# Kernel optimization log

Measured on AMD Instinct MI355X. Metric: run time of the kernel, lower is better.

Reference implementation:

```python
import jax, jax.numpy as jnp
import numpy as np

B, C, P, L = 128, 5, 5, 5
D = 128
USER_NUM, TITLE_NUM, ENTITY_NUM, REL_NUM = 50000, 30000, 100000, 100


def setup_inputs() -> dict:
    key = jax.random.key(0)
    k = jax.random.split(key, 22)
    f = jnp.float32
    s = 0.1  # weight scale to keep LSTM gates in a sane range
    return {
        "candidate_newsindex": jax.random.randint(k[0], (B, C), 0, TITLE_NUM),
        "user_index": jax.random.randint(k[1], (B,), 0, USER_NUM),
        "total_paths_index": jax.random.randint(k[2], (USER_NUM, C, P, L), 0, TITLE_NUM),
        "total_type_index": jax.random.randint(k[3], (USER_NUM, C, P, L), 0, 3),
        "total_relations_index": jax.random.randint(k[4], (USER_NUM, C, P, L), 0, REL_NUM),
        "entity_emb": jax.random.normal(k[5], (ENTITY_NUM, D), f),
        "relation_emb": jax.random.normal(k[6], (REL_NUM, D), f),
        "user_emb": jax.random.normal(k[7], (USER_NUM, D), f),
        "news_emb": jax.random.normal(k[8], (TITLE_NUM, D), f),
        "type_emb": jax.random.normal(k[9], (3, D), f),
        "Wih0": jax.random.normal(k[10], (P, 4 * D, 3 * D), f) * s,
        "Whh0": jax.random.normal(k[11], (P, 4 * D, D), f) * s,
        "bih0": jax.random.normal(k[12], (P, 4 * D), f) * s,
        "bhh0": jax.random.normal(k[13], (P, 4 * D), f) * s,
        "Wih1": jax.random.normal(k[14], (P, 4 * D, D), f) * s,
        "Whh1": jax.random.normal(k[15], (P, 4 * D, D), f) * s,
        "bih1": jax.random.normal(k[16], (P, 4 * D), f) * s,
        "bhh1": jax.random.normal(k[17], (P, 4 * D), f) * s,
        "W1": jax.random.normal(k[18], (16, D), f) * s,
        "b1": jax.random.normal(k[19], (16,), f) * s,
        "W2": jax.random.normal(k[20], (1, 16), f) * s,
        "b2": jax.random.normal(k[21], (1,), f) * s,
    }


def _lstm2(x, Wih0, Whh0, bih0, bhh0, Wih1, Whh1, bih1, bhh1):
    """2-layer PyTorch-style LSTM (gate order i,f,g,o). x: [N, T, in] -> [N, T, H]."""
    def layer(x, Wih, Whh, bih, bhh):
        N = x.shape[0]
        H = Whh.shape[1]
        h0 = jnp.zeros((N, H), x.dtype)
        c0 = jnp.zeros((N, H), x.dtype)
        b = bih + bhh
        def step(carry, xt):
            h, c = carry
            g = xt @ Wih.T + h @ Whh.T + b
            i, f, gg, o = jnp.split(g, 4, axis=-1)
            c = jax.nn.sigmoid(f) * c + jax.nn.sigmoid(i) * jnp.tanh(gg)
            h = jax.nn.sigmoid(o) * jnp.tanh(c)
            return (h, c), h
        _, ys = jax.lax.scan(step, (h0, c0), x.swapaxes(0, 1))
        return ys.swapaxes(0, 1)
    x = layer(x, Wih0, Whh0, bih0, bhh0)
    x = layer(x, Wih1, Whh1, bih1, bhh1)
    return x


def reference(candidate_newsindex, user_index, total_paths_index, total_type_index,
              total_relations_index, entity_emb, relation_emb, user_emb, news_emb,
              type_emb, Wih0, Whh0, bih0, bhh0, Wih1, Whh1, bih1, bhh1,
              W1, b1, W2, b2):
    bpath = total_paths_index[user_index]  # [B,C,P,L]
    btype = total_type_index[user_index]
    brel = total_relations_index[user_index]
    # per-node embedding selected by type: 0->user, 1->news, else entity
    node = jnp.where((btype == 0)[..., None], user_emb[bpath],
                     jnp.where((btype == 1)[..., None], news_emb[bpath], entity_emb[bpath]))
    inp = jnp.concatenate([node, type_emb[btype], relation_emb[brel]], axis=-1)  # [B,C,P,L,3D]
    Bb, Cc, Pp, Ll, F = inp.shape
    x = inp.transpose(2, 0, 1, 3, 4).reshape(Pp, Bb * Cc, Ll, F)  # per-path batches
    outs = jax.vmap(_lstm2)(x, Wih0, Whh0, bih0, bhh0, Wih1, Whh1, bih1, bhh1)  # [P,BC,L,H]
    idx = jnp.arange(Pp)
    sel = outs[idx, :, idx, :]  # LSTM i's output at timestep i -> [P, BC, H]
    ps = jax.nn.sigmoid(jnp.maximum(sel @ W1.T + b1, 0.0) @ W2.T + b2)[..., 0]  # [P,BC]
    ps_mean = ps.reshape(Pp, Bb, Cc).mean(axis=0)  # [B,C]
    # faithful to source: total_output accumulates over candidates j, so the score
    # for candidate j is the cumulative mean of path scores for candidates 0..j
    total_score = jnp.cumsum(ps_mean, axis=1) / jnp.arange(1, Cc + 1, dtype=ps_mean.dtype)
    emb_score = jax.nn.sigmoid(jnp.sum(news_emb[candidate_newsindex] * user_emb[user_index][:, None, :], axis=-1))
    return emb_score + total_score
```

## Files before the change

kernel.cpp:

```cpp
#include <hip/hip_runtime.h>
#include <math.h>

#define BB   128
#define CC   5
#define PP   5
#define LL   5
#define DD   128
#define NSEQ 640
#define GATES 512
#define IN0  384
#define HPAD 136

typedef __attribute__((ext_vector_type(8))) short short8;
typedef __attribute__((ext_vector_type(4))) float f32x4;

__device__ __forceinline__ float sigf(float x){ return 1.0f/(1.0f+__expf(-x)); }
__device__ __forceinline__ float tanhfast(float x){ return 1.0f - 2.0f/(__expf(2.0f*x)+1.0f); }

__device__ __forceinline__ unsigned short f2bf(float x){
    union { float f; unsigned u; } v; v.f = x;
    unsigned r = v.u + 0x7FFF + ((v.u >> 16) & 1);
    return (unsigned short)(r >> 16);
}

__device__ __constant__ int c_ptmap[15] = {0,5,6,10,11,12,15,16,17,18,20,21,22,23,24};

__global__ void stage0_kernel(const float* __restrict__ Wih0, const float* __restrict__ Whh0,
                              const float* __restrict__ Wih1, const float* __restrict__ Whh1,
                              const float* __restrict__ bih0, const float* __restrict__ bhh0,
                              const float* __restrict__ bih1, const float* __restrict__ bhh1,
                              unsigned short* __restrict__ F0, unsigned short* __restrict__ F1,
                              unsigned short* __restrict__ F2, unsigned short* __restrict__ F3,
                              float* __restrict__ b0, float* __restrict__ b1c,
                              float* __restrict__ psum,
                              const int* __restrict__ user_index,
                              const int* __restrict__ tpath, const int* __restrict__ ttype,
                              const int* __restrict__ trel,
                              const float* __restrict__ entity_emb, const float* __restrict__ relation_emb,
                              const float* __restrict__ user_emb, const float* __restrict__ news_emb,
                              const float* __restrict__ type_emb,
                              unsigned short* __restrict__ X){
    int bx = blockIdx.x;
    if (bx < 985){
        int id = bx*256 + threadIdx.x;
        const int NF0 = PP*12*32*64;
        const int NFH = PP*4*32*64;
        if (id < NF0 + 3*NFH){
            const float* src; unsigned short* dst; int K, KT, fid;
            if (id < NF0){ src = Wih0; dst = F0; K = IN0; KT = 12; fid = id; }
            else {
                int j = id - NF0; int m = j / NFH; fid = j % NFH; K = DD; KT = 4;
                src = (m==0)?Whh0:(m==1)?Wih1:Whh1;
                dst = (m==0)?F1:(m==1)?F2:F3;
            }
            int lane = fid & 63; int rem = fid >> 6;
            int gt = rem & 31; rem >>= 5;
            int kt = rem % KT; int p = rem / KT;
            int g  = gt*16 + (lane & 15);
            int k0 = kt*32 + (lane >> 4)*8;
            const float* s = src + (size_t)(p*GATES + g)*K + k0;
            float4 x0 = *(const float4*)s;
            float4 x1 = *(const float4*)(s+4);
            uint4 o;
            o.x = f2bf(x0.x) | ((unsigned)f2bf(x0.y)<<16);
            o.y = f2bf(x0.z) | ((unsigned)f2bf(x0.w)<<16);
            o.z = f2bf(x1.x) | ((unsigned)f2bf(x1.y)<<16);
            o.w = f2bf(x1.z) | ((unsigned)f2bf(x1.w)<<16);
            *(uint4*)(dst + (size_t)fid*8) = o;
        } else {
            int j = id - (NF0 + 3*NFH);
            if (j < PP*GATES) b0[j] = bih0[j] + bhh0[j];
            else if (j < 2*PP*GATES){ int q = j - PP*GATES; b1c[q] = bih1[q] + bhh1[q]; }
            else if (j < 2*PP*GATES + NSEQ){ psum[j - 2*PP*GATES] = 0.0f; }
        }
    } else {
        int id = (bx - 985)*256 + threadIdx.x;
        if (id >= 15*NSEQ*48) return;
        int ptIdx = id / (NSEQ*48); int rem = id % (NSEQ*48);
        int n = rem / 48, q = rem % 48;
        int pt = c_ptmap[ptIdx];
        int p = pt / LL, t = pt % LL;
        int b = n / CC, c = n % CC;
        int u = user_index[b];
        int base = ((u*CC + c)*PP + p)*LL + t;
        int col = q*8;
        const float* s;
        if (q < 16){
            int ty = ttype[base]; int pi = tpath[base];
            const float* e = (ty==0)?user_emb:(ty==1)?news_emb:entity_emb;
            s = e + (size_t)pi*DD + col;
        } else if (q < 32){
            s = type_emb + (size_t)ttype[base]*DD + (col-128);
        } else {
            s = relation_emb + (size_t)trel[base]*DD + (col-256);
        }
        float4 x0 = *(const float4*)s, x1 = *(const float4*)(s+4);
        uint4 o;
        o.x = f2bf(x0.x) | ((unsigned)f2bf(x0.y)<<16);
        o.y = f2bf(x0.z) | ((unsigned)f2bf(x0.w)<<16);
        o.z = f2bf(x1.x) | ((unsigned)f2bf(x1.y)<<16);
        o.w = f2bf(x1.z) | ((unsigned)f2bf(x1.w)<<16);
        *(uint4*)(X + (size_t)(pt*NSEQ + n)*IN0 + col) = o;
    }
}

__global__ __launch_bounds__(256) void gemm_ih0_v5(const unsigned short* __restrict__ X,
                                                   const unsigned short* __restrict__ F0,
                                                   float* __restrict__ G0c){
    __shared__ unsigned short Bs[12*4*512];
    int bx = blockIdx.x;
    int nch = bx & 7;
    int m64 = (bx >> 3) % 10;
    int pt  = c_ptmap[bx / 80];
    int p = pt / LL;
    int tid = threadIdx.x, lane = tid & 63, w = tid >> 6;
    int r16 = lane & 15, qd = lane >> 4;

    const unsigned short* Fp = F0 + (((size_t)p*12)*32 + nch*4)*512;
    uint4 breg[12];
    #pragma unroll
    for (int j=0;j<12;j++)
        breg[j] = *(const uint4*)(Fp + (size_t)j*32*512 + tid*8);
    #pragma unroll
    for (int j=0;j<12;j++)
        *(uint4*)(Bs + j*2048 + tid*8) = breg[j];
    __syncthreads();

    f32x4 acc[4];
    #pragma unroll
    for (int i=0;i<4;i++) acc[i] = (f32x4)0.0f;
    const unsigned short* Xb = X + ((size_t)pt*NSEQ + m64*64 + w*16 + r16)*IN0 + qd*8;
    #pragma unroll
    for (int kt=0; kt<12; kt++){
        short8 a = *(const short8*)(Xb + kt*32);
        #pragma unroll
        for (int i=0;i<4;i++){
            short8 bfr = *(const short8*)(Bs + (kt*4+i)*512 + lane*8);
            acc[i] = __builtin_amdgcn_mfma_f32_16x16x32_bf16(a, bfr, acc[i], 0,0,0);
        }
    }
    int tile16 = pt*40 + m64*4 + w;
    float* dst = G0c + (((size_t)tile16*32 + nch*4)*64 + lane)*4;
    #pragma unroll
    for (int i=0;i<4;i++)
        *(f32x4*)(dst + (size_t)i*256) = acc[i];
}

__global__ __launch_bounds__(512) void lstm_v5(
    const float* __restrict__ G0c,
    const unsigned short* __restrict__ F1,
    const unsigned short* __restrict__ F2,
    const unsigned short* __restrict__ F3,
    const float* __restrict__ b0, const float* __restrict__ b1c,
    const float* __restrict__ W1, const float* __restrict__ b1v,
    const float* __restrict__ W2, const float* __restrict__ b2v,
    float* __restrict__ psum){
    __shared__ unsigned short h0T[16*HPAD];
    __shared__ unsigned short h1T[16*HPAD];
    __shared__ float h1f[16*132];
    __shared__ float mlpb[16*17];

    int p = blockIdx.x / 40, nt = blockIdx.x % 40;
    int n0 = nt*16;
    int tid = threadIdx.x;
    int lane = tid & 63, w = tid >> 6;
    int r16 = lane & 15, qd = lane >> 4;
    int j = w*16 + r16;

    short8 f2r[16], f3r[16];
    {
        const unsigned short* F2p = F2 + (size_t)p*4*32*512 + lane*8;
        const unsigned short* F3p = F3 + (size_t)p*4*32*512 + lane*8;
        #pragma unroll
        for (int kt=0; kt<4; kt++)
            #pragma unroll
            for (int i=0;i<4;i++){
                f2r[kt*4+i] = *(const short8*)(F2p + (size_t)(kt*32 + i*8 + w)*512);
                f3r[kt*4+i] = *(const short8*)(F3p + (size_t)(kt*32 + i*8 + w)*512);
            }
    }
    float bL0[4], bL1[4];
    #pragma unroll
    for (int i=0;i<4;i++){
        int col = (i*8 + w)*16 + r16;
        bL0[i] = b0[p*GATES + col];
        bL1[i] = b1c[p*GATES + col];
    }
    const unsigned short* F1p = F1 + (size_t)p*4*32*512 + lane*8;

    f32x4 pf[4];
    {
        const float* slab = G0c + (size_t)((p*LL + 0)*40 + nt)*8192;
        #pragma unroll
        for (int i=0;i<4;i++) pf[i] = *(const f32x4*)(slab + ((i*8+w)*64 + lane)*4);
    }
    float c0s[4] = {0,0,0,0}, c1s[4] = {0,0,0,0};

    for (int t=0; t<=p; t++){
        f32x4 acc[4];
        #pragma unroll
        for (int i=0;i<4;i++){
            f32x4 a = pf[i]; float bb = bL0[i];
            a[0]+=bb; a[1]+=bb; a[2]+=bb; a[3]+=bb; acc[i]=a;
        }
        if (t < p){
            const float* ns = G0c + (size_t)((p*LL + t + 1)*40 + nt)*8192;
            #pragma unroll
            for (int i=0;i<4;i++) pf[i] = *(const f32x4*)(ns + ((i*8+w)*64 + lane)*4);
        }
        if (t > 0){
            #pragma unroll
            for (int kt=0; kt<4; kt++){
                short8 a = *(const short8*)(h0T + r16*HPAD + kt*32 + qd*8);
                #pragma unroll
                for (int i=0;i<4;i++){
                    short8 bfr = *(const short8*)(F1p + (size_t)(kt*32 + i*8 + w)*512);
                    acc[i] = __builtin_amdgcn_mfma_f32_16x16x32_bf16(a, bfr, acc[i], 0,0,0);
                }
            }
        }
        __syncthreads();
        #pragma unroll
        for (int v=0; v<4; v++){
            float cc = sigf(acc[1][v])*c0s[v] + sigf(acc[0][v])*tanhfast(acc[2][v]);
            c0s[v] = cc;
            h0T[(qd*4+v)*HPAD + j] = f2bf(sigf(acc[3][v])*tanhfast(cc));
        }
        __syncthreads();
        #pragma unroll
        for (int i=0;i<4;i++){
            float bb = bL1[i];
            f32x4 a; a[0]=bb; a[1]=bb; a[2]=bb; a[3]=bb; acc[i]=a;
        }
        #pragma unroll
        for (int kt=0; kt<4; kt++){
            short8 a = *(const short8*)(h0T + r16*HPAD + kt*32 + qd*8);
            #pragma unroll
            for (int i=0;i<4;i++)
                acc[i] = __builtin_amdgcn_mfma_f32_16x16x32_bf16(a, f2r[kt*4+i], acc[i], 0,0,0);
        }
        if (t > 0){
            #pragma unroll
            for (int kt=0; kt<4; kt++){
                short8 a = *(const short8*)(h1T + r16*HPAD + kt*32 + qd*8);
                #pragma unroll
                for (int i=0;i<4;i++)
                    acc[i] = __builtin_amdgcn_mfma_f32_16x16x32_bf16(a, f3r[kt*4+i], acc[i], 0,0,0);
            }
        }
        __syncthreads();
        #pragma unroll
        for (int v=0; v<4; v++){
            float cc = sigf(acc[1][v])*c1s[v] + sigf(acc[0][v])*tanhfast(acc[2][v]);
            c1s[v] = cc;
            float hh = sigf(acc[3][v])*tanhfast(cc);
            if (t < p) h1T[(qd*4+v)*HPAD + j] = f2bf(hh);
            else       h1f[(qd*4+v)*132 + j] = hh;
        }
    }
    __syncthreads();
    if (tid < 256){
        int rr = tid & 15, hc = tid >> 4;
        const float* w1r = W1 + hc*DD;
        float acc = b1v[hc];
        #pragma unroll 4
        for (int k=0;k<DD;k++) acc = fmaf(h1f[rr*132 + k], w1r[k], acc);
        mlpb[hc*17 + rr] = fmaxf(acc, 0.0f);
    }
    __syncthreads();
    if (tid < 16){
        float s = b2v[0];
        #pragma unroll
        for (int h=0;h<16;h++) s = fmaf(mlpb[h*17 + tid], W2[h], s);
        atomicAdd(&psum[n0 + tid], 0.2f*sigf(s));
    }
}

__global__ void final_kernel(const int* __restrict__ cand, const int* __restrict__ user_index,
                             const float* __restrict__ news_emb, const float* __restrict__ user_emb,
                             const float* __restrict__ psum, float* __restrict__ out){
    int b = blockIdx.x;
    int lane = threadIdx.x;
    int u = user_index[b];
    const float* ue = user_emb + (size_t)u*DD;
    float cum = 0.0f;
    for (int c=0;c<CC;c++){
        int nb = cand[b*CC + c];
        const float* ne = news_emb + (size_t)nb*DD;
        float v = ne[lane]*ue[lane] + ne[lane+64]*ue[lane+64];
        #pragma unroll
        for (int off=32; off; off>>=1) v += __shfl_down(v, off, 64);
        if (lane == 0){
            cum += psum[b*CC + c];
            out[b*CC + c] = sigf(v) + cum/(float)(c+1);
        }
    }
}

extern "C" void kernel_launch(void* const* d_in, const int* in_sizes, int n_in,
                              void* d_out, int out_size, void* d_ws, size_t ws_size,
                              hipStream_t stream){
    const int* cand        = (const int*)d_in[0];
    const int* uidx        = (const int*)d_in[1];
    const int* tpath       = (const int*)d_in[2];
    const int* ttype       = (const int*)d_in[3];
    const int* trel        = (const int*)d_in[4];
    const float* entity_emb   = (const float*)d_in[5];
    const float* relation_emb = (const float*)d_in[6];
    const float* user_emb     = (const float*)d_in[7];
    const float* news_emb     = (const float*)d_in[8];
    const float* type_emb     = (const float*)d_in[9];
    const float* Wih0 = (const float*)d_in[10];
    const float* Whh0 = (const float*)d_in[11];
    const float* bih0 = (const float*)d_in[12];
    const float* bhh0 = (const float*)d_in[13];
    const float* Wih1 = (const float*)d_in[14];
    const float* Whh1 = (const float*)d_in[15];
    const float* bih1 = (const float*)d_in[16];
    const float* bhh1 = (const float*)d_in[17];
    const float* W1 = (const float*)d_in[18];
    const float* b1 = (const float*)d_in[19];
    const float* W2 = (const float*)d_in[20];
    const float* b2 = (const float*)d_in[21];
    float* out = (float*)d_out;

    char* ws = (char*)d_ws;
    unsigned short* F0 = (unsigned short*)ws;  ws += (size_t)PP*12*32*512*2;
    unsigned short* F1 = (unsigned short*)ws;  ws += (size_t)PP*4*32*512*2;
    unsigned short* F2 = (unsigned short*)ws;  ws += (size_t)PP*4*32*512*2;
    unsigned short* F3 = (unsigned short*)ws;  ws += (size_t)PP*4*32*512*2;
    float* b0  = (float*)ws;                   ws += PP*GATES*4;
    float* b1c = (float*)ws;                   ws += PP*GATES*4;
    unsigned short* X = (unsigned short*)ws;   ws += (size_t)PP*LL*NSEQ*IN0*2;
    float* G0c = (float*)ws;                   ws += (size_t)PP*LL*NSEQ*GATES*4;
    float* psum = (float*)ws;                  ws += NSEQ*4;

    stage0_kernel<<<985+1800,256,0,stream>>>(Wih0,Whh0,Wih1,Whh1,bih0,bhh0,bih1,bhh1,
                                             F0,F1,F2,F3,b0,b1c,psum,
                                             uidx,tpath,ttype,trel,entity_emb,relation_emb,
                                             user_emb,news_emb,type_emb,X);
    gemm_ih0_v5<<<1200,256,0,stream>>>(X, F0, G0c);
    lstm_v5<<<200,512,0,stream>>>(G0c, F1, F2, F3, b0, b1c, W1, b1, W2, b2, psum);
    final_kernel<<<BB,64,0,stream>>>(cand, uidx, news_emb, user_emb, psum, out);
}
```

Before: 233.9 us.

## Double-buffer LSTM hidden state, cache F1 in registers, fuse final kernel

Result: slower. 351.2 us (+50.1%).

```diff
diff --git a/kernel.cpp b/kernel.cpp
--- a/kernel.cpp
+++ b/kernel.cpp
@@ -32,7 +32,7 @@
                               unsigned short* __restrict__ F0, unsigned short* __restrict__ F1,
                               unsigned short* __restrict__ F2, unsigned short* __restrict__ F3,
                               float* __restrict__ b0, float* __restrict__ b1c,
-                              float* __restrict__ psum,
+                              float* __restrict__ psum, unsigned* __restrict__ donecnt,
                               const int* __restrict__ user_index,
                               const int* __restrict__ tpath, const int* __restrict__ ttype,
                               const int* __restrict__ trel,
@@ -72,6 +72,7 @@
             if (j < PP*GATES) b0[j] = bih0[j] + bhh0[j];
             else if (j < 2*PP*GATES){ int q = j - PP*GATES; b1c[q] = bih1[q] + bhh1[q]; }
             else if (j < 2*PP*GATES + NSEQ){ psum[j - 2*PP*GATES] = 0.0f; }
+            else if (j == 2*PP*GATES + NSEQ){ *donecnt = 0u; }
         }
     } else {
         int id = (bx - 985)*256 + threadIdx.x;
@@ -146,7 +147,7 @@
         *(f32x4*)(dst + (size_t)i*256) = acc[i];
 }
 
-__global__ __launch_bounds__(512) void lstm_v5(
+__global__ __launch_bounds__(512) void lstm_v6(
     const float* __restrict__ G0c,
     const unsigned short* __restrict__ F1,
     const unsigned short* __restrict__ F2,
@@ -154,11 +155,15 @@
     const float* __restrict__ b0, const float* __restrict__ b1c,
     const float* __restrict__ W1, const float* __restrict__ b1v,
     const float* __restrict__ W2, const float* __restrict__ b2v,
-    float* __restrict__ psum){
-    __shared__ unsigned short h0T[16*HPAD];
-    __shared__ unsigned short h1T[16*HPAD];
+    float* __restrict__ psum, unsigned* __restrict__ donecnt,
+    const int* __restrict__ cand, const int* __restrict__ user_index,
+    const float* __restrict__ news_emb, const float* __restrict__ user_emb,
+    float* __restrict__ out){
+    __shared__ unsigned short h0T[2][16*HPAD];
+    __shared__ unsigned short h1T[2][16*HPAD];
     __shared__ float h1f[16*132];
     __shared__ float mlpb[16*17];
+    __shared__ int lastFlag;
 
     int p = blockIdx.x / 40, nt = blockIdx.x % 40;
     int n0 = nt*16;
@@ -167,14 +172,16 @@
     int r16 = lane & 15, qd = lane >> 4;
     int j = w*16 + r16;
 
-    short8 f2r[16], f3r[16];
+    short8 f1r[16], f2r[16], f3r[16];
     {
+        const unsigned short* F1p = F1 + (size_t)p*4*32*512 + lane*8;
         const unsigned short* F2p = F2 + (size_t)p*4*32*512 + lane*8;
         const unsigned short* F3p = F3 + (size_t)p*4*32*512 + lane*8;
         #pragma unroll
         for (int kt=0; kt<4; kt++)
             #pragma unroll
             for (int i=0;i<4;i++){
+                f1r[kt*4+i] = *(const short8*)(F1p + (size_t)(kt*32 + i*8 + w)*512);
                 f2r[kt*4+i] = *(const short8*)(F2p + (size_t)(kt*32 + i*8 + w)*512);
                 f3r[kt*4+i] = *(const short8*)(F3p + (size_t)(kt*32 + i*8 + w)*512);
             }
@@ -186,7 +193,6 @@
         bL0[i] = b0[p*GATES + col];
         bL1[i] = b1c[p*GATES + col];
     }
-    const unsigned short* F1p = F1 + (size_t)p*4*32*512 + lane*8;
 
     f32x4 pf[4];
     {
@@ -197,6 +203,7 @@
     float c0s[4] = {0,0,0,0}, c1s[4] = {0,0,0,0};
 
     for (int t=0; t<=p; t++){
+        int cur = t & 1, prv = cur ^ 1;
         f32x4 acc[4];
         #pragma unroll
         for (int i=0;i<4;i++){
@@ -211,20 +218,17 @@
         if (t > 0){
             #pragma unroll
             for (int kt=0; kt<4; kt++){
-                short8 a = *(const short8*)(h0T + r16*HPAD + kt*32 + qd*8);
+                short8 a = *(const short8*)(h0T[prv] + r16*HPAD + kt*32 + qd*8);
                 #pragma unroll
-                for (int i=0;i<4;i++){
-                    short8 bfr = *(const short8*)(F1p + (size_t)(kt*32 + i*8 + w)*512);
-                    acc[i] = __builtin_amdgcn_mfma_f32_16x16x32_bf16(a, bfr, acc[i], 0,0,0);
-                }
-            }
-        }
-        __syncthreads();
+                for (int i=0;i<4;i++)
+                    acc[i] = __builtin_amdgcn_mfma_f32_16x16x32_bf16(a, f1r[kt*4+i], acc[i], 0,0,0);
+            }
+        }
         #pragma unroll
         for (int v=0; v<4; v++){
             float cc = sigf(acc[1][v])*c0s[v] + sigf(acc[0][v])*tanhfast(acc[2][v]);
             c0s[v] = cc;
-            h0T[(qd*4+v)*HPAD + j] = f2bf(sigf(acc[3][v])*tanhfast(cc));
+            h0T[cur][(qd*4+v)*HPAD + j] = f2bf(sigf(acc[3][v])*tanhfast(cc));
         }
         __syncthreads();
         #pragma unroll
@@ -234,7 +238,7 @@
         }
         #pragma unroll
         for (int kt=0; kt<4; kt++){
-            short8 a = *(const short8*)(h0T + r16*HPAD + kt*32 + qd*8);
+            short8 a = *(const short8*)(h0T[cur] + r16*HPAD + kt*32 + qd*8);
             #pragma unroll
             for (int i=0;i<4;i++)
                 acc[i] = __builtin_amdgcn_mfma_f32_16x16x32_bf16(a, f2r[kt*4+i], acc[i], 0,0,0);
@@ -242,23 +246,22 @@
         if (t > 0){
             #pragma unroll
             for (int kt=0; kt<4; kt++){
-                short8 a = *(const short8*)(h1T + r16*HPAD + kt*32 + qd*8);
+                short8 a = *(const short8*)(h1T[prv] + r16*HPAD + kt*32 + qd*8);
                 #pragma unroll
                 for (int i=0;i<4;i++)
                     acc[i] = __builtin_amdgcn_mfma_f32_16x16x32_bf16(a, f3r[kt*4+i], acc[i], 0,0,0);
             }
         }
-        __syncthreads();
         #pragma unroll
         for (int v=0; v<4; v++){
             float cc = sigf(acc[1][v])*c1s[v] + sigf(acc[0][v])*tanhfast(acc[2][v]);
             c1s[v] = cc;
             float hh = sigf(acc[3][v])*tanhfast(cc);
-            if (t < p) h1T[(qd*4+v)*HPAD + j] = f2bf(hh);
+            if (t < p) h1T[cur][(qd*4+v)*HPAD + j] = f2bf(hh);
             else       h1f[(qd*4+v)*132 + j] = hh;
         }
-    }
-    __syncthreads();
+        __syncthreads();
+    }
     if (tid < 256){
         int rr = tid & 15, hc = tid >> 4;
         const float* w1r = W1 + hc*DD;
@@ -274,25 +277,30 @@
         for (int h=0;h<16;h++) s = fmaf(mlpb[h*17 + tid], W2[h], s);
         atomicAdd(&psum[n0 + tid], 0.2f*sigf(s));
     }
-}
-
-__global__ void final_kernel(const int* __restrict__ cand, const int* __restrict__ user_index,
-                             const float* __restrict__ news_emb, const float* __restrict__ user_emb,
-                             const float* __restrict__ psum, float* __restrict__ out){
-    int b = blockIdx.x;
-    int lane = threadIdx.x;
-    int u = user_index[b];
-    const float* ue = user_emb + (size_t)u*DD;
-    float cum = 0.0f;
-    for (int c=0;c<CC;c++){
-        int nb = cand[b*CC + c];
-        const float* ne = news_emb + (size_t)nb*DD;
-        float v = ne[lane]*ue[lane] + ne[lane+64]*ue[lane+64];
-        #pragma unroll
-        for (int off=32; off; off>>=1) v += __shfl_down(v, off, 64);
-        if (lane == 0){
-            cum += psum[b*CC + c];
-            out[b*CC + c] = sigf(v) + cum/(float)(c+1);
+    __threadfence();
+    __syncthreads();
+    if (tid == 0){
+        unsigned old = atomicAdd(donecnt, 1u);
+        lastFlag = (old == 199u) ? 1 : 0;
+    }
+    __syncthreads();
+    if (lastFlag){
+        for (int bi=0; bi<16; bi++){
+            int b = w*16 + bi;
+            int u = user_index[b];
+            const float* ue = user_emb + (size_t)u*DD;
+            float cum = 0.0f;
+            for (int c=0;c<CC;c++){
+                int nb = cand[b*CC + c];
+                const float* ne = news_emb + (size_t)nb*DD;
+                float v = ne[lane]*ue[lane] + ne[lane+64]*ue[lane+64];
+                #pragma unroll
+                for (int off=32; off; off>>=1) v += __shfl_down(v, off, 64);
+                if (lane == 0){
+                    cum += atomicAdd(&psum[b*CC + c], 0.0f);
+                    out[b*CC + c] = sigf(v) + cum/(float)(c+1);
+                }
+            }
         }
     }
 }
@@ -334,12 +342,13 @@
     unsigned short* X = (unsigned short*)ws;   ws += (size_t)PP*LL*NSEQ*IN0*2;
     float* G0c = (float*)ws;                   ws += (size_t)PP*LL*NSEQ*GATES*4;
     float* psum = (float*)ws;                  ws += NSEQ*4;
+    unsigned* donecnt = (unsigned*)ws;         ws += 64;
 
     stage0_kernel<<<985+1800,256,0,stream>>>(Wih0,Whh0,Wih1,Whh1,bih0,bhh0,bih1,bhh1,
-                                             F0,F1,F2,F3,b0,b1c,psum,
+                                             F0,F1,F2,F3,b0,b1c,psum,donecnt,
                                              uidx,tpath,ttype,trel,entity_emb,relation_emb,
                                              user_emb,news_emb,type_emb,X);
     gemm_ih0_v5<<<1200,256,0,stream>>>(X, F0, G0c);
-    lstm_v5<<<200,512,0,stream>>>(G0c, F1, F2, F3, b0, b1c, W1, b1, W2, b2, psum);
-    final_kernel<<<BB,64,0,stream>>>(cand, uidx, news_emb, user_emb, psum, out);
-}
+    lstm_v6<<<200,512,0,stream>>>(G0c, F1, F2, F3, b0, b1c, W1, b1, W2, b2,
+                                  psum, donecnt, cand, uidx, news_emb, user_emb, out);
+}
```

## Double-buffer LSTM hidden-state LDS and keep Whh0 fragments in registers

Applied to the files above, without the earlier changes.

Measured after the change: 235.9 us. No clear change (+0.8%).

```diff
diff --git a/kernel.cpp b/kernel.cpp
--- a/kernel.cpp
+++ b/kernel.cpp
@@ -146,7 +146,7 @@
         *(f32x4*)(dst + (size_t)i*256) = acc[i];
 }
 
-__global__ __launch_bounds__(512) void lstm_v5(
+__global__ __launch_bounds__(512, 2) void lstm_v7(
     const float* __restrict__ G0c,
     const unsigned short* __restrict__ F1,
     const unsigned short* __restrict__ F2,
@@ -155,8 +155,8 @@
     const float* __restrict__ W1, const float* __restrict__ b1v,
     const float* __restrict__ W2, const float* __restrict__ b2v,
     float* __restrict__ psum){
-    __shared__ unsigned short h0T[16*HPAD];
-    __shared__ unsigned short h1T[16*HPAD];
+    __shared__ unsigned short h0T[2][16*HPAD];
+    __shared__ unsigned short h1T[2][16*HPAD];
     __shared__ float h1f[16*132];
     __shared__ float mlpb[16*17];
 
@@ -167,14 +167,16 @@
     int r16 = lane & 15, qd = lane >> 4;
     int j = w*16 + r16;
 
-    short8 f2r[16], f3r[16];
+    short8 f1r[16], f2r[16], f3r[16];
     {
+        const unsigned short* F1p = F1 + (size_t)p*4*32*512 + lane*8;
         const unsigned short* F2p = F2 + (size_t)p*4*32*512 + lane*8;
         const unsigned short* F3p = F3 + (size_t)p*4*32*512 + lane*8;
         #pragma unroll
         for (int kt=0; kt<4; kt++)
             #pragma unroll
             for (int i=0;i<4;i++){
+                f1r[kt*4+i] = *(const short8*)(F1p + (size_t)(kt*32 + i*8 + w)*512);
                 f2r[kt*4+i] = *(const short8*)(F2p + (size_t)(kt*32 + i*8 + w)*512);
                 f3r[kt*4+i] = *(const short8*)(F3p + (size_t)(kt*32 + i*8 + w)*512);
             }
@@ -186,7 +188,6 @@
         bL0[i] = b0[p*GATES + col];
         bL1[i] = b1c[p*GATES + col];
     }
-    const unsigned short* F1p = F1 + (size_t)p*4*32*512 + lane*8;
 
     f32x4 pf[4];
     {
@@ -197,6 +198,7 @@
     float c0s[4] = {0,0,0,0}, c1s[4] = {0,0,0,0};
 
     for (int t=0; t<=p; t++){
+        int cur = t & 1, prv = cur ^ 1;
         f32x4 acc[4];
         #pragma unroll
         for (int i=0;i<4;i++){
@@ -211,20 +213,17 @@
         if (t > 0){
             #pragma unroll
             for (int kt=0; kt<4; kt++){
-                short8 a = *(const short8*)(h0T + r16*HPAD + kt*32 + qd*8);
+                short8 a = *(const short8*)(h0T[prv] + r16*HPAD + kt*32 + qd*8);
                 #pragma unroll
-                for (int i=0;i<4;i++){
-                    short8 bfr = *(const short8*)(F1p + (size_t)(kt*32 + i*8 + w)*512);
-                    acc[i] = __builtin_amdgcn_mfma_f32_16x16x32_bf16(a, bfr, acc[i], 0,0,0);
-                }
+                for (int i=0;i<4;i++)
+                    acc[i] = __builtin_amdgcn_mfma_f32_16x16x32_bf16(a, f1r[kt*4+i], acc[i], 0,0,0);
             }
         }
-        __syncthreads();
         #pragma unroll
         for (int v=0; v<4; v++){
             float cc = sigf(acc[1][v])*c0s[v] + sigf(acc[0][v])*tanhfast(acc[2][v]);
             c0s[v] = cc;
-            h0T[(qd*4+v)*HPAD + j] = f2bf(sigf(acc[3][v])*tanhfast(cc));
+            h0T[cur][(qd*4+v)*HPAD + j] = f2bf(sigf(acc[3][v])*tanhfast(cc));
         }
         __syncthreads();
         #pragma unroll
@@ -234,7 +233,7 @@
         }
         #pragma unroll
         for (int kt=0; kt<4; kt++){
-            short8 a = *(const short8*)(h0T + r16*HPAD + kt*32 + qd*8);
+            short8 a = *(const short8*)(h0T[cur] + r16*HPAD + kt*32 + qd*8);
             #pragma unroll
             for (int i=0;i<4;i++)
                 acc[i] = __builtin_amdgcn_mfma_f32_16x16x32_bf16(a, f2r[kt*4+i], acc[i], 0,0,0);
@@ -242,23 +241,22 @@
         if (t > 0){
             #pragma unroll
             for (int kt=0; kt<4; kt++){
-                short8 a = *(const short8*)(h1T + r16*HPAD + kt*32 + qd*8);
+                short8 a = *(const short8*)(h1T[prv] + r16*HPAD + kt*32 + qd*8);
                 #pragma unroll
                 for (int i=0;i<4;i++)
                     acc[i] = __builtin_amdgcn_mfma_f32_16x16x32_bf16(a, f3r[kt*4+i], acc[i], 0,0,0);
             }
         }
-        __syncthreads();
         #pragma unroll
         for (int v=0; v<4; v++){
             float cc = sigf(acc[1][v])*c1s[v] + sigf(acc[0][v])*tanhfast(acc[2][v]);
             c1s[v] = cc;
             float hh = sigf(acc[3][v])*tanhfast(cc);
-            if (t < p) h1T[(qd*4+v)*HPAD + j] = f2bf(hh);
+            if (t < p) h1T[cur][(qd*4+v)*HPAD + j] = f2bf(hh);
             else       h1f[(qd*4+v)*132 + j] = hh;
         }
-    }
-    __syncthreads();
+        __syncthreads();
+    }
     if (tid < 256){
         int rr = tid & 15, hc = tid >> 4;
         const float* w1r = W1 + hc*DD;
@@ -340,6 +338,6 @@
                                              uidx,tpath,ttype,trel,entity_emb,relation_emb,
                                              user_emb,news_emb,type_emb,X);
     gemm_ih0_v5<<<1200,256,0,stream>>>(X, F0, G0c);
-    lstm_v5<<<200,512,0,stream>>>(G0c, F1, F2, F3, b0, b1c, W1, b1, W2, b2, psum);
+    lstm_v7<<<200,512,0,stream>>>(G0c, F1, F2, F3, b0, b1c, W1, b1, W2, b2, psum);
     final_kernel<<<BB,64,0,stream>>>(cand, uidx, news_emb, user_emb, psum, out);
 }
```
